# Kernel tuning notes

Measured on AMD Instinct MI355X. Metric: run time of the kernel, lower is better.

## Reference

```python
import jax, jax.numpy as jnp
import numpy as np

B, NBAND, C, T = 2, 40, 64, 1500
NUM_CODE = 1024


def setup_inputs() -> dict:
    key = jax.random.key(0)
    k1, k2 = jax.random.split(key)
    x = jax.random.normal(k1, (B, NBAND, C, T), dtype=jnp.float32)
    # layer_idx == 0 init: unit-norm codes per band
    cb = jax.random.normal(k2, (NBAND, NUM_CODE, C), dtype=jnp.float32)
    eps = jnp.finfo(jnp.float32).eps
    cb = cb / jnp.sqrt(jnp.sum(cb * cb, axis=-1, keepdims=True) + eps)
    return {"x": x, "codebook": cb}


def reference(x, codebook):
    batch, nband, nchan, time = x.shape
    num_code = codebook.shape[1]
    # x.detach().permute(0,3,1,2).view(B*T, nband, nchan)
    xd = jax.lax.stop_gradient(x).transpose(0, 3, 1, 2).reshape(batch * time, nband, nchan)
    dist = (
        jnp.sum(xd * xd, axis=-1, keepdims=True)
        + jnp.sum(codebook * codebook, axis=-1)
        - 2.0 * jnp.einsum("nbc,bkc->nbk", xd, codebook)
    )
    min_idx = jnp.argmin(dist, axis=-1)  # [BT, nband]
    # per-band gather: quantized[n, b] = codebook[b, min_idx[n, b]]
    quantized = codebook[jnp.arange(nband)[None, :], min_idx]  # [BT, nband, nchan]
    # view(B, T, nband, nchan).permute(0,2,3,1)
    return quantized.reshape(batch, time, nband, nchan).transpose(0, 2, 3, 1)
```

## Files before the change

kernel.cpp:

```cpp
#include <hip/hip_runtime.h>


#define NBAND  40
#define CH     64
#define TT     1500
#define NCODE  1024
#define MT     128
#define PAD    68
#define THRESH 1e-3f

typedef short v8s __attribute__((ext_vector_type(8)));
typedef float v4f __attribute__((ext_vector_type(4)));

#define CBF_USHORTS ((size_t)NBAND * 32 * 8 * 64 * 8)
#define CBF_BYTES   (CBF_USHORTS * 2)
#define WS_NEEDED   (CBF_BYTES + (size_t)NBAND * NCODE * 4)

__device__ __forceinline__ unsigned short f2bf(float f) {
    unsigned u = __float_as_uint(f);
    return (unsigned short)((u + 0x7FFFu + ((u >> 16) & 1u)) >> 16);
}
__device__ __forceinline__ float bf2f(unsigned short h) {
    return __uint_as_float(((unsigned)h) << 16);
}
__device__ __forceinline__ unsigned ford(float f) {
    unsigned u = __float_as_uint(f);
    return (u & 0x80000000u) ? ~u : (u | 0x80000000u);
}
__device__ __forceinline__ unsigned long long packsk(float f, unsigned k) {
    return ((unsigned long long)ford(f) << 32) | (unsigned long long)k;
}
__device__ __forceinline__ float med3f(float a, float b, float c) {
#if __has_builtin(__builtin_amdgcn_fmed3f)
    return __builtin_amdgcn_fmed3f(a, b, c);
#else
    return fminf(fmaxf(a, b), c);
#endif
}

__global__ __launch_bounds__(256)
void vq_prep(const float* __restrict__ cb,
             unsigned short* __restrict__ CBF,
             float* __restrict__ C2) {
    const int band = blockIdx.y;
    const int g    = blockIdx.x * 4 + (threadIdx.x >> 6);
    const int lane = threadIdx.x & 63;
    const int col  = lane & 15;
    const int quad = lane >> 4;

    float sq[2] = {0.f, 0.f};
    #pragma unroll
    for (int l = 0; l < 4; ++l) {
        const int ni = l >> 1, ks = l & 1;
        const int code = g * 32 + ni * 16 + col;
        const int c0   = ks * 32 + quad * 8;
        const float* src = cb + ((size_t)(band * NCODE + code)) * CH + c0;
        const float4 v0 = *(const float4*)src;
        const float4 v1 = *(const float4*)(src + 4);
        const float vv[8] = {v0.x, v0.y, v0.z, v0.w, v1.x, v1.y, v1.z, v1.w};
        union { unsigned short u[8]; v8s v; } hh, ll;
        #pragma unroll
        for (int j = 0; j < 8; ++j) {
            const unsigned short h = f2bf(vv[j]);
            hh.u[j] = h;
            ll.u[j] = f2bf(vv[j] - bf2f(h));
            sq[ni] = fmaf(vv[j], vv[j], sq[ni]);
        }
        const size_t gb = (size_t)(band * 32 + g) * 8;
        *(v8s*)&CBF[(gb + l)     * 512 + lane * 8] = hh.v;
        *(v8s*)&CBF[(gb + 4 + l) * 512 + lane * 8] = ll.v;
    }
    #pragma unroll
    for (int ni = 0; ni < 2; ++ni) {
        sq[ni] += __shfl_xor(sq[ni], 16);
        sq[ni] += __shfl_xor(sq[ni], 32);
    }
    if (quad == 0) {
        C2[band * NCODE + g * 32 + col]      = sq[0];
        C2[band * NCODE + g * 32 + 16 + col] = sq[1];
    }
}

__global__ __launch_bounds__(256, 3)
void vq_main(const float* __restrict__ x,
             const float* __restrict__ cb,
             const unsigned short* __restrict__ CBF,
             const float* __restrict__ C2f,
             float* __restrict__ out) {
    __shared__ alignas(16) unsigned char SMEM[MT * PAD * 2 * 2];
    __shared__ float c2_s[NCODE];
    __shared__ unsigned long long best_s[MT];
    __shared__ unsigned amb_s[4];
    __shared__ float xrow_s[CH];

    unsigned short* XH_s = (unsigned short*)SMEM;
    unsigned short* XL_s = XH_s + MT * PAD;

    const int tile  = blockIdx.x;
    const int band  = blockIdx.y;
    const int batch = blockIdx.z;
    const int t0    = tile * MT;

    const int tid  = threadIdx.x;
    const int wave = tid >> 6;
    const int lane = tid & 63;
    const int quad = lane >> 4;
    const int col  = lane & 15;

    if (tid < 4) amb_s[tid] = 0u;
    {
        const float* src = C2f + band * NCODE;
        #pragma unroll
        for (int i = 0; i < 4; ++i) c2_s[tid + 256 * i] = src[tid + 256 * i];
    }
    {
        const int c = tid & 63;
        const int g = tid >> 6;
        const float* src = x + ((size_t)(batch * NBAND + band) * CH + c) * TT + t0;
        #pragma unroll
        for (int i = 0; i < 8; ++i) {
            const int t = (g + 4 * i) * 4;
            float4 v = make_float4(0.f, 0.f, 0.f, 0.f);
            if (t0 + t + 3 < TT) v = *(const float4*)(src + t);
            const float vv[4] = {v.x, v.y, v.z, v.w};
            #pragma unroll
            for (int j = 0; j < 4; ++j) {
                const unsigned short h = f2bf(vv[j]);
                XH_s[(t + j) * PAD + c] = h;
                XL_s[(t + j) * PAD + c] = f2bf(vv[j] - bf2f(h));
            }
        }
    }
    __syncthreads();

    v8s ah[2][2], al[2][2];
    #pragma unroll
    for (int mi = 0; mi < 2; ++mi)
        #pragma unroll
        for (int ks = 0; ks < 2; ++ks) {
            const int off = (wave * 32 + mi * 16 + col) * PAD + ks * 32 + quad * 8;
            ah[mi][ks] = *(const v8s*)&XH_s[off];
            al[mi][ks] = *(const v8s*)&XL_s[off];
        }
    __syncthreads();

    float m1[8], m2[8];
    int   id8[8];
    #pragma unroll
    for (int i = 0; i < 8; ++i) { m1[i] = 3.4028235e38f; m2[i] = 3.4028235e38f; id8[i] = 0x7fffffff; }

    const unsigned short* fb = CBF + (size_t)(band * 32) * 4096 + (size_t)lane * 8;

    auto compute = [&](const v8s (&buf)[8], int g) {
        v4f acc[2][2];
        #pragma unroll
        for (int mi = 0; mi < 2; ++mi)
            #pragma unroll
            for (int ni = 0; ni < 2; ++ni) acc[mi][ni] = (v4f){0.f, 0.f, 0.f, 0.f};
        #pragma unroll
        for (int ks = 0; ks < 2; ++ks) {
            const v8s bh0 = buf[0 * 2 + ks], bh1 = buf[2 + ks];
            const v8s bl0 = buf[4 + ks],     bl1 = buf[6 + ks];
            #pragma unroll
            for (int mi = 0; mi < 2; ++mi) {
                acc[mi][0] = __builtin_amdgcn_mfma_f32_16x16x32_bf16(ah[mi][ks], bh0, acc[mi][0], 0, 0, 0);
                acc[mi][1] = __builtin_amdgcn_mfma_f32_16x16x32_bf16(ah[mi][ks], bh1, acc[mi][1], 0, 0, 0);
            }
            #pragma unroll
            for (int mi = 0; mi < 2; ++mi) {
                acc[mi][0] = __builtin_amdgcn_mfma_f32_16x16x32_bf16(ah[mi][ks], bl0, acc[mi][0], 0, 0, 0);
                acc[mi][1] = __builtin_amdgcn_mfma_f32_16x16x32_bf16(ah[mi][ks], bl1, acc[mi][1], 0, 0, 0);
            }
            #pragma unroll
            for (int mi = 0; mi < 2; ++mi) {
                acc[mi][0] = __builtin_amdgcn_mfma_f32_16x16x32_bf16(al[mi][ks], bh0, acc[mi][0], 0, 0, 0);
                acc[mi][1] = __builtin_amdgcn_mfma_f32_16x16x32_bf16(al[mi][ks], bh1, acc[mi][1], 0, 0, 0);
            }
        }
        #pragma unroll
        for (int ni = 0; ni < 2; ++ni) {
            const float c2v = c2_s[g * 32 + ni * 16 + col];
            const int   kg  = g * 32 + ni * 16 + col;
            #pragma unroll
            for (int mi = 0; mi < 2; ++mi)
                #pragma unroll
                for (int r = 0; r < 4; ++r) {
                    const int j = mi * 4 + r;
                    const float s = fmaf(-2.f, acc[mi][ni][r], c2v);
                    m2[j] = med3f(s, m1[j], m2[j]);
                    const bool lt = s < m1[j];
                    m1[j]  = lt ? s : m1[j];
                    id8[j] = lt ? kg : id8[j];
                }
        }
    };

    v8s bufA[8], bufB[8];
    #pragma unroll
    for (int p = 0; p < 8; ++p) bufA[p] = *(const v8s*)(fb + p * 512);

    for (int g = 0; g < 32; g += 2) {
        const unsigned short* nf = fb + (size_t)(g + 1) * 4096;
        #pragma unroll
        for (int p = 0; p < 8; ++p) bufB[p] = *(const v8s*)(nf + p * 512);
        compute(bufA, g);
        if (g + 2 < 32) {
            const unsigned short* nf2 = fb + (size_t)(g + 2) * 4096;
            #pragma unroll
            for (int p = 0; p < 8; ++p) bufA[p] = *(const v8s*)(nf2 + p * 512);
        }
        compute(bufB, g + 1);
    }
    __syncthreads();

    float* RM1 = (float*)SMEM;
    float* RM2 = RM1 + MT * 16;
    int*   RI  = (int*)(RM2 + MT * 16);
    #pragma unroll
    for (int j = 0; j < 8; ++j) {
        const int t = wave * 32 + (j >> 2) * 16 + quad * 4 + (j & 3);
        RM1[t * 16 + col] = m1[j];
        RM2[t * 16 + col] = m2[j];
        RI [t * 16 + col] = id8[j];
    }
    __syncthreads();

    if (tid < MT) {
        const int t = tid;
        float M1 = RM1[t * 16], M2 = RM2[t * 16];
        int   I  = RI[t * 16];
        #pragma unroll
        for (int j = 1; j < 16; ++j) {
            const float a1 = RM1[t * 16 + j];
            const float a2 = RM2[t * 16 + j];
            const int   ai = RI [t * 16 + j];
            if (a1 < M1 || (a1 == M1 && ai < I)) { M2 = fminf(M2, M1); M1 = a1; I = ai; }
            else                                  { M2 = fminf(M2, a1); }
            M2 = fminf(M2, a2);
        }
        best_s[t] = packsk(M1, (unsigned)I);
        if ((M2 - M1) <= THRESH && t0 + t < TT)
            atomicOr(&amb_s[t >> 5], 1u << (t & 31));
    }
    __syncthreads();

    for (int t = 0; t < MT; ++t) {
        if ((amb_s[t >> 5] >> (t & 31)) & 1u) {
            if (tid < CH) xrow_s[tid] = x[((size_t)(batch * NBAND + band) * CH + tid) * TT + t0 + t];
            if (tid == CH) best_s[t] = ~0ULL;
            __syncthreads();
            #pragma unroll
            for (int i = 0; i < 4; ++i) {
                const int k = tid * 4 + i;
                const float* crow = cb + ((size_t)(band * NCODE + k)) * CH;
                float dot = 0.f, c2e = 0.f;
                #pragma unroll 8
                for (int c = 0; c < CH; ++c) {
                    const float cv = crow[c];
                    dot = fmaf(cv, xrow_s[c], dot);
                    c2e = fmaf(cv, cv, c2e);
                }
                atomicMin(&best_s[t], packsk(fmaf(-2.f, dot, c2e), (unsigned)k));
            }
            __syncthreads();
        }
    }
    __syncthreads();

    {
        float* OT = (float*)SMEM;
        #pragma unroll
        for (int r = 0; r < MT; r += 4) {
            const int row = r + wave;
            const unsigned idx = (unsigned)(best_s[row] & 0xFFFFFFFFull) & (NCODE - 1);
            OT[row * 67 + lane] = cb[((size_t)(band * NCODE + idx)) * CH + lane];
        }
        __syncthreads();
        const int tloc  = tid & 127;
        const int chalf = tid >> 7;
        if (t0 + tloc < TT) {
            float* ob = out + ((size_t)(batch * NBAND + band) * CH) * TT + t0 + tloc;
            #pragma unroll
            for (int i = 0; i < 32; ++i) {
                const int c = chalf * 32 + i;
                ob[(size_t)c * TT] = OT[tloc * 67 + c];
            }
        }
    }
}

#define TN 128
#define KC 128
__global__ __launch_bounds__(256, 2)
void vq_fp32_kernel(const float* __restrict__ x,
                    const float* __restrict__ cb,
                    float* __restrict__ out) {
    __shared__ float XT_s[CH * TN];
    __shared__ float CBT_s[CH * KC];
    __shared__ float c2part[256];
    const int tile = blockIdx.x, band = blockIdx.y, batch = blockIdx.z;
    const int t0 = tile * TN;
    const int tid = threadIdx.x;
    const int tx = tid & 15, ty = tid >> 4;
    {
        const int c = tid >> 2, q = tid & 3;
        const float* src = x + ((size_t)(batch * NBAND + band) * CH + c) * TT + t0;
        #pragma unroll
        for (int i = 0; i < 8; ++i) {
            const int t = q * 32 + i * 4;
            float4 v = make_float4(0.f, 0.f, 0.f, 0.f);
            if (t0 + t < TT) v = *(const float4*)(src + t);
            *(float4*)&XT_s[c * TN + t] = v;
        }
    }
    float vmin[8]; int vidx[8];
    #pragma unroll
    for (int i = 0; i < 8; ++i) { vmin[i] = 3.4e38f; vidx[i] = 0x7fffffff; }
    for (int kc = 0; kc < NCODE; kc += KC) {
        __syncthreads();
        {
            const int k = tid >> 1, ch0 = (tid & 1) * 32;
            const float* src = cb + ((size_t)(band * NCODE + kc + k)) * CH + ch0;
            float s = 0.f;
            #pragma unroll
            for (int i = 0; i < 8; ++i) {
                const float4 v = *(const float4*)(src + i * 4);
                const int c0 = ch0 + i * 4;
                CBT_s[(c0 + 0) * KC + k] = v.x; CBT_s[(c0 + 1) * KC + k] = v.y;
                CBT_s[(c0 + 2) * KC + k] = v.z; CBT_s[(c0 + 3) * KC + k] = v.w;
                s = fmaf(v.x, v.x, s); s = fmaf(v.y, v.y, s);
                s = fmaf(v.z, v.z, s); s = fmaf(v.w, v.w, s);
            }
            c2part[tid] = s;
        }
        __syncthreads();
        float acc[8][8];
        #pragma unroll
        for (int ii = 0; ii < 8; ++ii)
            #pragma unroll
            for (int jj = 0; jj < 8; ++jj) acc[ii][jj] = 0.f;
        #pragma unroll 4
        for (int c = 0; c < CH; ++c) {
            const float4 xa0 = *(const float4*)&XT_s[c * TN + tx * 4];
            const float4 xa1 = *(const float4*)&XT_s[c * TN + 64 + tx * 4];
            const float4 cv0 = *(const float4*)&CBT_s[c * KC + ty * 4];
            const float4 cv1 = *(const float4*)&CBT_s[c * KC + 64 + ty * 4];
            const float xa[8] = {xa0.x, xa0.y, xa0.z, xa0.w, xa1.x, xa1.y, xa1.z, xa1.w};
            const float cv[8] = {cv0.x, cv0.y, cv0.z, cv0.w, cv1.x, cv1.y, cv1.z, cv1.w};
            #pragma unroll
            for (int ii = 0; ii < 8; ++ii)
                #pragma unroll
                for (int jj = 0; jj < 8; ++jj) acc[ii][jj] = fmaf(xa[ii], cv[jj], acc[ii][jj]);
        }
        #pragma unroll
        for (int jj = 0; jj < 8; ++jj) {
            const int kl = (jj < 4) ? (ty * 4 + jj) : (64 + ty * 4 + (jj - 4));
            const float c2v = c2part[2 * kl] + c2part[2 * kl + 1];
            const int kglob = kc + kl;
            #pragma unroll
            for (int ii = 0; ii < 8; ++ii) {
                const float score = fmaf(-2.f, acc[ii][jj], c2v);
                if (score < vmin[ii]) { vmin[ii] = score; vidx[ii] = kglob; }
            }
        }
    }
    __syncthreads();
    float* redv = XT_s;
    int* redi = (int*)(XT_s + TN * 16);
    int* idxs = (int*)(XT_s + TN * 32);
    #pragma unroll
    for (int ii = 0; ii < 8; ++ii) {
        const int t = (ii < 4) ? (tx * 4 + ii) : (64 + tx * 4 + (ii - 4));
        redv[t * 16 + ty] = vmin[ii];
        redi[t * 16 + ty] = vidx[ii];
    }
    __syncthreads();
    if (tid < TN) {
        float bv = redv[tid * 16]; int bi = redi[tid * 16];
        #pragma unroll
        for (int j = 1; j < 16; ++j) {
            const float v = redv[tid * 16 + j]; const int id = redi[tid * 16 + j];
            if (v < bv || (v == bv && id < bi)) { bv = v; bi = id; }
        }
        idxs[tid] = bi;
    }
    __syncthreads();
    {
        const int tloc = tid & 127, chalf = tid >> 7;
        if (t0 + tloc < TT) {
            const int idx = idxs[tloc];
            const float* crow = cb + ((size_t)(band * NCODE + idx)) * CH;
            float* ob = out + ((size_t)(batch * NBAND + band) * CH) * TT + t0 + tloc;
            #pragma unroll
            for (int i = 0; i < 32; ++i) {
                const int c = chalf * 32 + i;
                ob[(size_t)c * TT] = crow[c];
            }
        }
    }
}

extern "C" void kernel_launch(void* const* d_in, const int* in_sizes, int n_in,
                              void* d_out, int out_size, void* d_ws, size_t ws_size,
                              hipStream_t stream) {
    const float* x  = (const float*)d_in[0];
    const float* cb = (const float*)d_in[1];
    float* out = (float*)d_out;
    dim3 grid((TT + MT - 1) / MT, NBAND, 2);
    if (ws_size >= WS_NEEDED) {
        unsigned short* CBF = (unsigned short*)d_ws;
        float* C2 = (float*)((char*)d_ws + CBF_BYTES);
        vq_prep<<<dim3(8, NBAND), dim3(256), 0, stream>>>(cb, CBF, C2);
        vq_main<<<grid, dim3(256), 0, stream>>>(x, cb, CBF, C2, out);
    } else {
        vq_fp32_kernel<<<grid, dim3(256), 0, stream>>>(x, cb, out);
    }
}
```

Before: 216.3 us.

## Halve time tile, split codebook across waves, stage codebook via async LDS loads

The time tile shrinks from 128 to 64 rows, and the four waves now split as two time-halves by two codebook-halves. Each pair of waves shares codebook fragments that are loaded into LDS with double-buffered global_load_lds instead of each wave streaming them into registers. The aim is to cut redundant global codebook traffic and register pressure, which allows four blocks per CU and twice as many blocks in the grid. In exchange it adds a barrier per round, a 32-way final reduction, and roughly double the total codebook reads across blocks.

```diff
diff --git a/kernel.cpp b/kernel.cpp
--- a/kernel.cpp
+++ b/kernel.cpp
@@ -5,7 +5,7 @@
 #define CH     64
 #define TT     1500
 #define NCODE  1024
-#define MT     128
+#define MT     64
 #define PAD    68
 #define THRESH 1e-3f
 
@@ -36,6 +36,12 @@
 #else
     return fminf(fmaxf(a, b), c);
 #endif
+}
+
+typedef __attribute__((address_space(1))) const unsigned char* gas_p;
+typedef __attribute__((address_space(3))) unsigned char*       las_p;
+__device__ __forceinline__ void async_ld16(const void* g, void* l) {
+    __builtin_amdgcn_global_load_lds((gas_p)g, (las_p)l, 16, 0, 0);
 }
 
 __global__ __launch_bounds__(256)
@@ -81,44 +87,45 @@
     }
 }
 
-__global__ __launch_bounds__(256, 3)
+__global__ __launch_bounds__(256, 4)
 void vq_main(const float* __restrict__ x,
              const float* __restrict__ cb,
              const unsigned short* __restrict__ CBF,
              const float* __restrict__ C2f,
              float* __restrict__ out) {
-    __shared__ alignas(16) unsigned char SMEM[MT * PAD * 2 * 2];
+    __shared__ alignas(16) unsigned char SMEM[32768];
     __shared__ float c2_s[NCODE];
     __shared__ unsigned long long best_s[MT];
-    __shared__ unsigned amb_s[4];
+    __shared__ unsigned amb_s[2];
     __shared__ float xrow_s[CH];
-
-    unsigned short* XH_s = (unsigned short*)SMEM;
-    unsigned short* XL_s = XH_s + MT * PAD;
 
     const int tile  = blockIdx.x;
     const int band  = blockIdx.y;
     const int batch = blockIdx.z;
     const int t0    = tile * MT;
 
-    const int tid  = threadIdx.x;
-    const int wave = tid >> 6;
-    const int lane = tid & 63;
-    const int quad = lane >> 4;
-    const int col  = lane & 15;
-
-    if (tid < 4) amb_s[tid] = 0u;
+    const int tid   = threadIdx.x;
+    const int wave  = tid >> 6;
+    const int lane  = tid & 63;
+    const int quad  = lane >> 4;
+    const int col   = lane & 15;
+    const int thalf = wave & 1;
+    const int khalf = wave >> 1;
+
+    if (tid < 2) amb_s[tid] = 0u;
     {
         const float* src = C2f + band * NCODE;
         #pragma unroll
         for (int i = 0; i < 4; ++i) c2_s[tid + 256 * i] = src[tid + 256 * i];
     }
     {
+        unsigned short* XH_s = (unsigned short*)SMEM;
+        unsigned short* XL_s = XH_s + MT * PAD;
         const int c = tid & 63;
         const int g = tid >> 6;
         const float* src = x + ((size_t)(batch * NBAND + band) * CH + c) * TT + t0;
         #pragma unroll
-        for (int i = 0; i < 8; ++i) {
+        for (int i = 0; i < 4; ++i) {
             const int t = (g + 4 * i) * 4;
             float4 v = make_float4(0.f, 0.f, 0.f, 0.f);
             if (t0 + t + 3 < TT) v = *(const float4*)(src + t);
@@ -134,14 +141,18 @@
     __syncthreads();
 
     v8s ah[2][2], al[2][2];
-    #pragma unroll
-    for (int mi = 0; mi < 2; ++mi)
-        #pragma unroll
-        for (int ks = 0; ks < 2; ++ks) {
-            const int off = (wave * 32 + mi * 16 + col) * PAD + ks * 32 + quad * 8;
-            ah[mi][ks] = *(const v8s*)&XH_s[off];
-            al[mi][ks] = *(const v8s*)&XL_s[off];
-        }
+    {
+        unsigned short* XH_s = (unsigned short*)SMEM;
+        unsigned short* XL_s = XH_s + MT * PAD;
+        #pragma unroll
+        for (int mi = 0; mi < 2; ++mi)
+            #pragma unroll
+            for (int ks = 0; ks < 2; ++ks) {
+                const int off = (thalf * 32 + mi * 16 + col) * PAD + ks * 32 + quad * 8;
+                ah[mi][ks] = *(const v8s*)&XH_s[off];
+                al[mi][ks] = *(const v8s*)&XL_s[off];
+            }
+    }
     __syncthreads();
 
     float m1[8], m2[8];
@@ -149,18 +160,39 @@
     #pragma unroll
     for (int i = 0; i < 8; ++i) { m1[i] = 3.4028235e38f; m2[i] = 3.4028235e38f; id8[i] = 0x7fffffff; }
 
-    const unsigned short* fb = CBF + (size_t)(band * 32) * 4096 + (size_t)lane * 8;
-
-    auto compute = [&](const v8s (&buf)[8], int g) {
+    unsigned short* LBUF = (unsigned short*)SMEM;
+    const unsigned short* cbase = CBF + (size_t)(band * 32) * 4096 + (size_t)lane * 8;
+    const int pbase = (thalf) * 4;
+
+    auto stage_round = [&](int r, int b) {
+        const int group = khalf * 16 + r;
+        #pragma unroll
+        for (int i = 0; i < 4; ++i) {
+            const int p = pbase + i;
+            async_ld16(cbase + (size_t)group * 4096 + p * 512,
+                       LBUF + (size_t)b * 8192 + khalf * 4096 + p * 512);
+        }
+    };
+
+    stage_round(0, 0);
+
+    for (int r = 0; r < 16; ++r) {
+        __syncthreads();
+        if (r + 1 < 16) stage_round(r + 1, (r + 1) & 1);
+
+        const unsigned short* lb = LBUF + (size_t)(r & 1) * 8192 + khalf * 4096 + lane * 8;
         v4f acc[2][2];
         #pragma unroll
         for (int mi = 0; mi < 2; ++mi)
             #pragma unroll
             for (int ni = 0; ni < 2; ++ni) acc[mi][ni] = (v4f){0.f, 0.f, 0.f, 0.f};
+
         #pragma unroll
         for (int ks = 0; ks < 2; ++ks) {
-            const v8s bh0 = buf[0 * 2 + ks], bh1 = buf[2 + ks];
-            const v8s bl0 = buf[4 + ks],     bl1 = buf[6 + ks];
+            const v8s bh0 = *(const v8s*)(lb + (0 + ks) * 512);
+            const v8s bh1 = *(const v8s*)(lb + (2 + ks) * 512);
+            const v8s bl0 = *(const v8s*)(lb + (4 + ks) * 512);
+            const v8s bl1 = *(const v8s*)(lb + (6 + ks) * 512);
             #pragma unroll
             for (int mi = 0; mi < 2; ++mi) {
                 acc[mi][0] = __builtin_amdgcn_mfma_f32_16x16x32_bf16(ah[mi][ks], bh0, acc[mi][0], 0, 0, 0);
@@ -179,61 +211,45 @@
         }
         #pragma unroll
         for (int ni = 0; ni < 2; ++ni) {
-            const float c2v = c2_s[g * 32 + ni * 16 + col];
-            const int   kg  = g * 32 + ni * 16 + col;
+            const int   kg  = khalf * 512 + r * 32 + ni * 16 + col;
+            const float c2v = c2_s[kg];
             #pragma unroll
             for (int mi = 0; mi < 2; ++mi)
                 #pragma unroll
-                for (int r = 0; r < 4; ++r) {
-                    const int j = mi * 4 + r;
-                    const float s = fmaf(-2.f, acc[mi][ni][r], c2v);
+                for (int rr = 0; rr < 4; ++rr) {
+                    const int j = mi * 4 + rr;
+                    const float s = fmaf(-2.f, acc[mi][ni][rr], c2v);
                     m2[j] = med3f(s, m1[j], m2[j]);
                     const bool lt = s < m1[j];
                     m1[j]  = lt ? s : m1[j];
                     id8[j] = lt ? kg : id8[j];
                 }
         }
-    };
-
-    v8s bufA[8], bufB[8];
-    #pragma unroll
-    for (int p = 0; p < 8; ++p) bufA[p] = *(const v8s*)(fb + p * 512);
-
-    for (int g = 0; g < 32; g += 2) {
-        const unsigned short* nf = fb + (size_t)(g + 1) * 4096;
-        #pragma unroll
-        for (int p = 0; p < 8; ++p) bufB[p] = *(const v8s*)(nf + p * 512);
-        compute(bufA, g);
-        if (g + 2 < 32) {
-            const unsigned short* nf2 = fb + (size_t)(g + 2) * 4096;
-            #pragma unroll
-            for (int p = 0; p < 8; ++p) bufA[p] = *(const v8s*)(nf2 + p * 512);
-        }
-        compute(bufB, g + 1);
     }
     __syncthreads();
 
     float* RM1 = (float*)SMEM;
-    float* RM2 = RM1 + MT * 16;
-    int*   RI  = (int*)(RM2 + MT * 16);
+    float* RM2 = RM1 + MT * 32;
+    int*   RI  = (int*)(RM2 + MT * 32);
     #pragma unroll
     for (int j = 0; j < 8; ++j) {
-        const int t = wave * 32 + (j >> 2) * 16 + quad * 4 + (j & 3);
-        RM1[t * 16 + col] = m1[j];
-        RM2[t * 16 + col] = m2[j];
-        RI [t * 16 + col] = id8[j];
+        const int t    = thalf * 32 + (j >> 2) * 16 + quad * 4 + (j & 3);
+        const int slot = khalf * 16 + col;
+        RM1[t * 32 + slot] = m1[j];
+        RM2[t * 32 + slot] = m2[j];
+        RI [t * 32 + slot] = id8[j];
     }
     __syncthreads();
 
     if (tid < MT) {
         const int t = tid;
-        float M1 = RM1[t * 16], M2 = RM2[t * 16];
-        int   I  = RI[t * 16];
-        #pragma unroll
-        for (int j = 1; j < 16; ++j) {
-            const float a1 = RM1[t * 16 + j];
-            const float a2 = RM2[t * 16 + j];
-            const int   ai = RI [t * 16 + j];
+        float M1 = RM1[t * 32], M2 = RM2[t * 32];
+        int   I  = RI[t * 32];
+        #pragma unroll 8
+        for (int j = 1; j < 32; ++j) {
+            const float a1 = RM1[t * 32 + j];
+            const float a2 = RM2[t * 32 + j];
+            const int   ai = RI [t * 32 + j];
             if (a1 < M1 || (a1 == M1 && ai < I)) { M2 = fminf(M2, M1); M1 = a1; I = ai; }
             else                                  { M2 = fminf(M2, a1); }
             M2 = fminf(M2, a2);
@@ -270,19 +286,19 @@
     {
         float* OT = (float*)SMEM;
         #pragma unroll
-        for (int r = 0; r < MT; r += 4) {
-            const int row = r + wave;
+        for (int rr = 0; rr < MT; rr += 4) {
+            const int row = rr + wave;
             const unsigned idx = (unsigned)(best_s[row] & 0xFFFFFFFFull) & (NCODE - 1);
             OT[row * 67 + lane] = cb[((size_t)(band * NCODE + idx)) * CH + lane];
         }
         __syncthreads();
-        const int tloc  = tid & 127;
-        const int chalf = tid >> 7;
+        const int tloc = tid & 63;
+        const int cq   = tid >> 6;
         if (t0 + tloc < TT) {
             float* ob = out + ((size_t)(batch * NBAND + band) * CH) * TT + t0 + tloc;
             #pragma unroll
-            for (int i = 0; i < 32; ++i) {
-                const int c = chalf * 32 + i;
+            for (int i = 0; i < 16; ++i) {
+                const int c = cq * 16 + i;
                 ob[(size_t)c * TT] = OT[tloc * 67 + c];
             }
         }
@@ -406,13 +422,14 @@
     const float* x  = (const float*)d_in[0];
     const float* cb = (const float*)d_in[1];
     float* out = (float*)d_out;
-    dim3 grid((TT + MT - 1) / MT, NBAND, 2);
     if (ws_size >= WS_NEEDED) {
         unsigned short* CBF = (unsigned short*)d_ws;
         float* C2 = (float*)((char*)d_ws + CBF_BYTES);
         vq_prep<<<dim3(8, NBAND), dim3(256), 0, stream>>>(cb, CBF, C2);
+        dim3 grid((TT + MT - 1) / MT, NBAND, 2);
         vq_main<<<grid, dim3(256), 0, stream>>>(x, cb, CBF, C2, out);
     } else {
+        dim3 grid((TT + TN - 1) / TN, NBAND, 2);
         vq_fp32_kernel<<<grid, dim3(256), 0, stream>>>(x, cb, out);
     }
 }
```

Result: faster. 205.4 us (-5.0%).
